# Kernel optimization log

Measured on AMD Instinct MI355X. Metric: run time of the kernel, lower is better.

## Reference

```python
import jax, jax.numpy as jnp
import numpy as np

RES = 2048
IN = 3
OUT = 2
THRESHOLD = 1.0
BETA = 0.9
SPECTRAL_RADIUS = 0.9


def _make_W(rng):
    # random recurrent matrix scaled to target spectral radius (power iteration estimate)
    W = rng.standard_normal((RES, RES)).astype(np.float32)
    v = rng.standard_normal(RES).astype(np.float32)
    lam = 1.0
    for _ in range(100):
        v = W @ v
        lam = np.linalg.norm(v)
        v = v / (lam + 1e-12)
    return W * (SPECTRAL_RADIUS / lam)


def _xavier(rng, fan_out, fan_in):
    bound = np.sqrt(6.0 / (fan_in + fan_out))
    return rng.uniform(-bound, bound, (fan_out, fan_in)).astype(np.float32)


def setup_inputs() -> dict:
    key = jax.random.key(0)
    rng = np.random.default_rng(42)
    x = jax.random.normal(key, (200, 256, IN), dtype=jnp.float32)
    W = jnp.asarray(_make_W(rng))            # [RES, RES] recurrent weights
    Win = jnp.asarray(_xavier(rng, RES, IN))  # [RES, IN]  input_layer.weight
    Wout = jnp.asarray(_xavier(rng, OUT, RES))  # [OUT, RES] readout.weight
    return {"x": x, "W": W, "Win": Win, "Wout": Wout}


def reference(x, W, Win, Wout):
    seq_len, batch, _ = x.shape
    res = W.shape[0]

    def step(carry, x_t):
        V, S = carry
        # leaky integrate: input current + recurrent current
        V_new = BETA * V + x_t @ Win.T + S @ W  # [batch, res]
        S_new = (V_new >= THRESHOLD).astype(V.dtype)
        V_new = V_new * (1.0 - S_new)  # reset_mechanism == 'zero'
        return (V_new, S_new), S_new

    init = (jnp.zeros((batch, res), x.dtype), jnp.zeros((batch, res), x.dtype))
    _, spk_rec = jax.lax.scan(step, init, x)  # [seq, batch, res]
    spk_avg = spk_rec[-10:].mean(axis=0)       # [batch, res]
    logits = spk_avg @ Wout.T                  # [batch, out]
    return spk_rec, logits
```

## Files before the change

kernel.cpp:

```cpp
#include <hip/hip_runtime.h>


#define SEQ    200
#define BATCH  256
#define NRES   2048
#define NTHR   1024
#define BETA_F 0.9f

__global__ __launch_bounds__(NTHR, 1) void snn_reservoir_kernel(
    const float* __restrict__ x,
    const float* __restrict__ W,
    const float* __restrict__ Win,
    const float* __restrict__ Wout,
    float* __restrict__ out)
{
    const int b    = blockIdx.x;
    const int tid  = threadIdx.x;
    const int lane = tid & 63;
    const int wid  = tid >> 6;
    const int n0   = tid << 1;

    __shared__ unsigned long long smask[2][32];
    __shared__ int   scum[2];
    __shared__ float4 sx[SEQ];
    __shared__ float red[2][16];

    for (int t = tid; t < SEQ; t += NTHR) {
        const float* p = x + (size_t)t * (BATCH * 3) + b * 3;
        sx[t] = make_float4(p[0], p[1], p[2], 0.0f);
    }
    if (tid < 64) smask[tid >> 5][tid & 31] = 0ull;
    if (tid < 2)  scum[tid] = 0;

    const float* wr = Win + (size_t)n0 * 3;
    const float w00 = wr[0], w01 = wr[1], w02 = wr[2];
    const float w10 = wr[3], w11 = wr[4], w12 = wr[5];

    float V0 = 0.f, V1 = 0.f;
    int cnt0 = 0, cnt1 = 0;

    __syncthreads();

    auto step = [&](int t, int cur, int prev, int& seen) {
        float rec0 = 0.f, rec1 = 0.f;
        const int c = scum[prev];
        if (__builtin_expect(c != seen, 0)) {
            seen = c;
            #pragma unroll 1
            for (int u = 0; u < 32; ++u) {
                unsigned long long m = smask[prev][u];
                const int kbase = ((u >> 1) << 7) + (u & 1);
                while (m) {
                    const int l = __builtin_ctzll(m);
                    m &= m - 1;
                    const int k = kbase + (l << 1);
                    const float2 wv = *(const float2*)(W + (size_t)k * NRES + n0);
                    rec0 += wv.x;
                    rec1 += wv.y;
                }
            }
        }
        const float4 xv = sx[t];
        const float i0 = fmaf(xv.x, w00, fmaf(xv.y, w01, xv.z * w02)) + rec0;
        const float i1 = fmaf(xv.x, w10, fmaf(xv.y, w11, xv.z * w12)) + rec1;
        V0 = fmaf(BETA_F, V0, i0);
        V1 = fmaf(BETA_F, V1, i1);
        const bool s0 = (V0 >= 1.0f);
        const bool s1 = (V1 >= 1.0f);
        V0 = s0 ? 0.f : V0;
        V1 = s1 ? 0.f : V1;
        *(float2*)(out + ((size_t)t * BATCH + b) * NRES + n0) =
            make_float2(s0 ? 1.f : 0.f, s1 ? 1.f : 0.f);
        if (t >= SEQ - 10) { cnt0 += (int)s0; cnt1 += (int)s1; }
        const unsigned long long b0 = __ballot(s0);
        const unsigned long long b1 = __ballot(s1);
        if (lane == 0) {
            smask[cur][2 * wid]     = b0;
            smask[cur][2 * wid + 1] = b1;
            const int pc = __popcll(b0) + __popcll(b1);
            if (pc) atomicAdd(&scum[cur], pc);
        }
        asm volatile("s_waitcnt lgkmcnt(0)\n\ts_barrier" ::: "memory");
    };

    int seen0 = 0, seen1 = 0;
    for (int tt = 0; tt < SEQ; tt += 2) {
        step(tt,     0, 1, seen1);
        step(tt + 1, 1, 0, seen0);
    }

    const float a0 = (float)cnt0 * 0.1f;
    const float a1 = (float)cnt1 * 0.1f;
    float p0 = fmaf(a0, Wout[n0], a1 * Wout[n0 + 1]);
    float p1 = fmaf(a0, Wout[NRES + n0], a1 * Wout[NRES + n0 + 1]);
    #pragma unroll
    for (int off = 32; off > 0; off >>= 1) {
        p0 += __shfl_down(p0, off);
        p1 += __shfl_down(p1, off);
    }
    if (lane == 0) { red[0][wid] = p0; red[1][wid] = p1; }
    __syncthreads();
    if (tid == 0) {
        float q0 = 0.f, q1 = 0.f;
        #pragma unroll
        for (int i = 0; i < 16; ++i) { q0 += red[0][i]; q1 += red[1][i]; }
        const size_t loff = (size_t)SEQ * BATCH * NRES;
        out[loff + b * 2 + 0] = q0;
        out[loff + b * 2 + 1] = q1;
    }
}

extern "C" void kernel_launch(void* const* d_in, const int* in_sizes, int n_in,
                              void* d_out, int out_size, void* d_ws, size_t ws_size,
                              hipStream_t stream) {
    const float* x    = (const float*)d_in[0];
    const float* W    = (const float*)d_in[1];
    const float* Win  = (const float*)d_in[2];
    const float* Wout = (const float*)d_in[3];
    float* out = (float*)d_out;
    hipLaunchKernelGGL(snn_reservoir_kernel, dim3(BATCH), dim3(NTHR), 0, stream,
                       x, W, Win, Wout, out);
}
```

Before: 410.2 us.

## Add barrier-free speculative no-spike pass with fallback to full recurrent simulation

Each block first runs the whole sequence ignoring recurrence, with no per-step barriers. This is exact as long as no neuron ever spikes, because the recurrent term is then zero. If any spike occurs, a block-wide flag triggers a re-run of the full simulation with per-step ballots, atomics and barriers, and it overwrites the output. Each thread now handles 4 neurons with float4 stores and gathers, on 512 threads per block. The aim is to remove the 200 per-step barriers when inputs never drive the membrane over threshold, at the cost of doing the work twice when they do.

```diff
diff --git a/kernel.cpp b/kernel.cpp
--- a/kernel.cpp
+++ b/kernel.cpp
@@ -4,7 +4,7 @@
 #define SEQ    200
 #define BATCH  256
 #define NRES   2048
-#define NTHR   1024
+#define NTHR   512
 #define BETA_F 0.9f
 
 __global__ __launch_bounds__(NTHR, 1) void snn_reservoir_kernel(
@@ -18,81 +18,125 @@
     const int tid  = threadIdx.x;
     const int lane = tid & 63;
     const int wid  = tid >> 6;
-    const int n0   = tid << 1;
+    const int n0   = tid << 2;
 
+    __shared__ float4 sx[SEQ];
     __shared__ unsigned long long smask[2][32];
     __shared__ int   scum[2];
-    __shared__ float4 sx[SEQ];
-    __shared__ float red[2][16];
+    __shared__ float red[2][8];
+    __shared__ int   anyflag;
 
     for (int t = tid; t < SEQ; t += NTHR) {
         const float* p = x + (size_t)t * (BATCH * 3) + b * 3;
         sx[t] = make_float4(p[0], p[1], p[2], 0.0f);
     }
-    if (tid < 64) smask[tid >> 5][tid & 31] = 0ull;
-    if (tid < 2)  scum[tid] = 0;
+    if (tid == 0) anyflag = 0;
 
-    const float* wr = Win + (size_t)n0 * 3;
-    const float w00 = wr[0], w01 = wr[1], w02 = wr[2];
-    const float w10 = wr[3], w11 = wr[4], w12 = wr[5];
+    float wi[4][3];
+    #pragma unroll
+    for (int j = 0; j < 4; ++j) {
+        const float* p = Win + (size_t)(n0 + j) * 3;
+        wi[j][0] = p[0]; wi[j][1] = p[1]; wi[j][2] = p[2];
+    }
 
-    float V0 = 0.f, V1 = 0.f;
-    int cnt0 = 0, cnt1 = 0;
+    float V[4]  = {0.f, 0.f, 0.f, 0.f};
+    int   cnt[4] = {0, 0, 0, 0};
 
     __syncthreads();
 
-    auto step = [&](int t, int cur, int prev, int& seen) {
-        float rec0 = 0.f, rec1 = 0.f;
-        const int c = scum[prev];
-        if (__builtin_expect(c != seen, 0)) {
-            seen = c;
-            #pragma unroll 1
-            for (int u = 0; u < 32; ++u) {
-                unsigned long long m = smask[prev][u];
-                const int kbase = ((u >> 1) << 7) + (u & 1);
-                while (m) {
-                    const int l = __builtin_ctzll(m);
-                    m &= m - 1;
-                    const int k = kbase + (l << 1);
-                    const float2 wv = *(const float2*)(W + (size_t)k * NRES + n0);
-                    rec0 += wv.x;
-                    rec1 += wv.y;
+    {
+        float* po = out + (size_t)b * NRES + n0;
+        bool spiked = false;
+        #pragma unroll 2
+        for (int t = 0; t < SEQ; ++t) {
+            const float4 xv = sx[t];
+            float4 sp;
+            #pragma unroll
+            for (int j = 0; j < 4; ++j) {
+                const float cur = fmaf(xv.x, wi[j][0],
+                                  fmaf(xv.y, wi[j][1], xv.z * wi[j][2]));
+                V[j] = fmaf(BETA_F, V[j], cur);
+                const bool s = (V[j] >= 1.0f);
+                spiked |= s;
+                V[j] = s ? 0.f : V[j];
+                ((float*)&sp)[j] = s ? 1.f : 0.f;
+                if (t >= SEQ - 10) cnt[j] += (int)s;
+            }
+            *(float4*)po = sp;
+            po += BATCH * NRES;
+        }
+        const unsigned long long bal = __ballot(spiked);
+        if (lane == 0 && bal != 0ull) atomicOr(&anyflag, 1);
+    }
+    __syncthreads();
+
+    if (anyflag) {
+        #pragma unroll
+        for (int j = 0; j < 4; ++j) { V[j] = 0.f; cnt[j] = 0; }
+        if (tid < 64) smask[tid >> 5][tid & 31] = 0ull;
+        if (tid < 2)  scum[tid] = 0;
+        __syncthreads();
+
+        int seen[2] = {0, 0};
+        float* po = out + (size_t)b * NRES + n0;
+        for (int t = 0; t < SEQ; ++t) {
+            const int curp = t & 1, prev = curp ^ 1;
+            float rec[4] = {0.f, 0.f, 0.f, 0.f};
+            const int c = scum[prev];
+            if (c != seen[prev]) {
+                seen[prev] = c;
+                #pragma unroll 1
+                for (int u = 0; u < 32; ++u) {
+                    unsigned long long m = smask[prev][u];
+                    const int kbase = ((u >> 2) << 8) + (u & 3);
+                    while (m) {
+                        const int l = __builtin_ctzll(m);
+                        m &= m - 1;
+                        const int k = kbase + (l << 2);
+                        const float4 wv = *(const float4*)(W + (size_t)k * NRES + n0);
+                        rec[0] += wv.x; rec[1] += wv.y;
+                        rec[2] += wv.z; rec[3] += wv.w;
+                    }
                 }
             }
+            const float4 xv = sx[t];
+            float4 sp;
+            int pc = 0;
+            unsigned long long bj[4];
+            #pragma unroll
+            for (int j = 0; j < 4; ++j) {
+                const float cur = fmaf(xv.x, wi[j][0],
+                                  fmaf(xv.y, wi[j][1], xv.z * wi[j][2])) + rec[j];
+                V[j] = fmaf(BETA_F, V[j], cur);
+                const bool s = (V[j] >= 1.0f);
+                V[j] = s ? 0.f : V[j];
+                ((float*)&sp)[j] = s ? 1.f : 0.f;
+                if (t >= SEQ - 10) cnt[j] += (int)s;
+                bj[j] = __ballot(s);
+                pc += (int)s;
+            }
+            *(float4*)po = sp;
+            po += BATCH * NRES;
+            if (lane == 0) {
+                #pragma unroll
+                for (int j = 0; j < 4; ++j) smask[curp][(wid << 2) + j] = bj[j];
+            }
+            if (lane == 0) {
+                int wpc = 0;
+                #pragma unroll
+                for (int j = 0; j < 4; ++j) wpc += __popcll(bj[j]);
+                if (wpc) atomicAdd(&scum[curp], wpc);
+            }
+            __syncthreads();
         }
-        const float4 xv = sx[t];
-        const float i0 = fmaf(xv.x, w00, fmaf(xv.y, w01, xv.z * w02)) + rec0;
-        const float i1 = fmaf(xv.x, w10, fmaf(xv.y, w11, xv.z * w12)) + rec1;
-        V0 = fmaf(BETA_F, V0, i0);
-        V1 = fmaf(BETA_F, V1, i1);
-        const bool s0 = (V0 >= 1.0f);
-        const bool s1 = (V1 >= 1.0f);
-        V0 = s0 ? 0.f : V0;
-        V1 = s1 ? 0.f : V1;
-        *(float2*)(out + ((size_t)t * BATCH + b) * NRES + n0) =
-            make_float2(s0 ? 1.f : 0.f, s1 ? 1.f : 0.f);
-        if (t >= SEQ - 10) { cnt0 += (int)s0; cnt1 += (int)s1; }
-        const unsigned long long b0 = __ballot(s0);
-        const unsigned long long b1 = __ballot(s1);
-        if (lane == 0) {
-            smask[cur][2 * wid]     = b0;
-            smask[cur][2 * wid + 1] = b1;
-            const int pc = __popcll(b0) + __popcll(b1);
-            if (pc) atomicAdd(&scum[cur], pc);
-        }
-        asm volatile("s_waitcnt lgkmcnt(0)\n\ts_barrier" ::: "memory");
-    };
-
-    int seen0 = 0, seen1 = 0;
-    for (int tt = 0; tt < SEQ; tt += 2) {
-        step(tt,     0, 1, seen1);
-        step(tt + 1, 1, 0, seen0);
     }
 
-    const float a0 = (float)cnt0 * 0.1f;
-    const float a1 = (float)cnt1 * 0.1f;
-    float p0 = fmaf(a0, Wout[n0], a1 * Wout[n0 + 1]);
-    float p1 = fmaf(a0, Wout[NRES + n0], a1 * Wout[NRES + n0 + 1]);
+    const float4 w0 = *(const float4*)(Wout + n0);
+    const float4 w1 = *(const float4*)(Wout + NRES + n0);
+    float p0 = cnt[0] * 0.1f * w0.x + cnt[1] * 0.1f * w0.y +
+               cnt[2] * 0.1f * w0.z + cnt[3] * 0.1f * w0.w;
+    float p1 = cnt[0] * 0.1f * w1.x + cnt[1] * 0.1f * w1.y +
+               cnt[2] * 0.1f * w1.z + cnt[3] * 0.1f * w1.w;
     #pragma unroll
     for (int off = 32; off > 0; off >>= 1) {
         p0 += __shfl_down(p0, off);
@@ -103,7 +147,7 @@
     if (tid == 0) {
         float q0 = 0.f, q1 = 0.f;
         #pragma unroll
-        for (int i = 0; i < 16; ++i) { q0 += red[0][i]; q1 += red[1][i]; }
+        for (int i = 0; i < 8; ++i) { q0 += red[0][i]; q1 += red[1][i]; }
         const size_t loff = (size_t)SEQ * BATCH * NRES;
         out[loff + b * 2 + 0] = q0;
         out[loff + b * 2 + 1] = q1;
```

New measurement: 423.7 us. +3.3%, slower.

## Add barrier-free speculative no-spike pass with fallback to full recurrent loop

Applied to the files above, without the earlier changes.

Runs a first pass that ignores the recurrent term, updates the membrane potentials with no per-step barrier and writes spikes with nontemporal stores. The recurrent contribution is only nonzero once some neuron has spiked, so if no thread in the block ever spikes this pass is exact. A block-wide flag detects any spike, and in that case the block reruns the original barrier-synchronised recurrent simulation from scratch. This removes 200 block barriers per step loop in the common no-spike case, at the cost of doubling the work and output writes for blocks that do spike.

```diff
diff --git a/kernel.cpp b/kernel.cpp
--- a/kernel.cpp
+++ b/kernel.cpp
@@ -6,6 +6,8 @@
 #define NRES   2048
 #define NTHR   1024
 #define BETA_F 0.9f
+
+typedef float f2_t __attribute__((ext_vector_type(2)));
 
 __global__ __launch_bounds__(NTHR, 1) void snn_reservoir_kernel(
     const float* __restrict__ x,
@@ -20,17 +22,17 @@
     const int wid  = tid >> 6;
     const int n0   = tid << 1;
 
+    __shared__ float4 sx[SEQ];
     __shared__ unsigned long long smask[2][32];
     __shared__ int   scum[2];
-    __shared__ float4 sx[SEQ];
     __shared__ float red[2][16];
+    __shared__ int   anyflag;
 
     for (int t = tid; t < SEQ; t += NTHR) {
         const float* p = x + (size_t)t * (BATCH * 3) + b * 3;
         sx[t] = make_float4(p[0], p[1], p[2], 0.0f);
     }
-    if (tid < 64) smask[tid >> 5][tid & 31] = 0ull;
-    if (tid < 2)  scum[tid] = 0;
+    if (tid == 0) anyflag = 0;
 
     const float* wr = Win + (size_t)n0 * 3;
     const float w00 = wr[0], w01 = wr[1], w02 = wr[2];
@@ -41,52 +43,87 @@
 
     __syncthreads();
 
-    auto step = [&](int t, int cur, int prev, int& seen) {
-        float rec0 = 0.f, rec1 = 0.f;
-        const int c = scum[prev];
-        if (__builtin_expect(c != seen, 0)) {
-            seen = c;
-            #pragma unroll 1
-            for (int u = 0; u < 32; ++u) {
-                unsigned long long m = smask[prev][u];
-                const int kbase = ((u >> 1) << 7) + (u & 1);
-                while (m) {
-                    const int l = __builtin_ctzll(m);
-                    m &= m - 1;
-                    const int k = kbase + (l << 1);
-                    const float2 wv = *(const float2*)(W + (size_t)k * NRES + n0);
-                    rec0 += wv.x;
-                    rec1 += wv.y;
+    {
+        float* po = out + (size_t)b * NRES + n0;
+        bool spiked = false;
+        #pragma unroll 4
+        for (int t = 0; t < SEQ - 10; ++t) {
+            const float4 xv = sx[t];
+            V0 = fmaf(BETA_F, V0, fmaf(xv.x, w00, fmaf(xv.y, w01, xv.z * w02)));
+            V1 = fmaf(BETA_F, V1, fmaf(xv.x, w10, fmaf(xv.y, w11, xv.z * w12)));
+            const bool s0 = (V0 >= 1.0f), s1 = (V1 >= 1.0f);
+            spiked |= (s0 | s1);
+            V0 = s0 ? 0.f : V0;
+            V1 = s1 ? 0.f : V1;
+            f2_t sp; sp[0] = s0 ? 1.f : 0.f; sp[1] = s1 ? 1.f : 0.f;
+            __builtin_nontemporal_store(sp, (f2_t*)po);
+            po += BATCH * NRES;
+        }
+        #pragma unroll
+        for (int t = SEQ - 10; t < SEQ; ++t) {
+            const float4 xv = sx[t];
+            V0 = fmaf(BETA_F, V0, fmaf(xv.x, w00, fmaf(xv.y, w01, xv.z * w02)));
+            V1 = fmaf(BETA_F, V1, fmaf(xv.x, w10, fmaf(xv.y, w11, xv.z * w12)));
+            const bool s0 = (V0 >= 1.0f), s1 = (V1 >= 1.0f);
+            spiked |= (s0 | s1);
+            cnt0 += (int)s0; cnt1 += (int)s1;
+            V0 = s0 ? 0.f : V0;
+            V1 = s1 ? 0.f : V1;
+            f2_t sp; sp[0] = s0 ? 1.f : 0.f; sp[1] = s1 ? 1.f : 0.f;
+            __builtin_nontemporal_store(sp, (f2_t*)po);
+            po += BATCH * NRES;
+        }
+        const unsigned long long bal = __ballot(spiked);
+        if (lane == 0 && bal != 0ull) atomicOr(&anyflag, 1);
+    }
+    __syncthreads();
+
+    if (anyflag) {
+        V0 = 0.f; V1 = 0.f; cnt0 = 0; cnt1 = 0;
+        if (tid < 64) smask[tid >> 5][tid & 31] = 0ull;
+        if (tid < 2)  scum[tid] = 0;
+        __syncthreads();
+
+        int seen[2] = {0, 0};
+        float* po = out + (size_t)b * NRES + n0;
+        for (int t = 0; t < SEQ; ++t) {
+            const int curp = t & 1, prev = curp ^ 1;
+            float rec0 = 0.f, rec1 = 0.f;
+            const int c = scum[prev];
+            if (c != seen[prev]) {
+                seen[prev] = c;
+                #pragma unroll 1
+                for (int u = 0; u < 32; ++u) {
+                    unsigned long long m = smask[prev][u];
+                    const int kbase = ((u >> 1) << 7) + (u & 1);
+                    while (m) {
+                        const int l = __builtin_ctzll(m);
+                        m &= m - 1;
+                        const int k = kbase + (l << 1);
+                        const float2 wv = *(const float2*)(W + (size_t)k * NRES + n0);
+                        rec0 += wv.x; rec1 += wv.y;
+                    }
                 }
             }
+            const float4 xv = sx[t];
+            V0 = fmaf(BETA_F, V0, fmaf(xv.x, w00, fmaf(xv.y, w01, xv.z * w02)) + rec0);
+            V1 = fmaf(BETA_F, V1, fmaf(xv.x, w10, fmaf(xv.y, w11, xv.z * w12)) + rec1);
+            const bool s0 = (V0 >= 1.0f), s1 = (V1 >= 1.0f);
+            V0 = s0 ? 0.f : V0;
+            V1 = s1 ? 0.f : V1;
+            *(float2*)po = make_float2(s0 ? 1.f : 0.f, s1 ? 1.f : 0.f);
+            po += BATCH * NRES;
+            if (t >= SEQ - 10) { cnt0 += (int)s0; cnt1 += (int)s1; }
+            const unsigned long long b0 = __ballot(s0);
+            const unsigned long long b1 = __ballot(s1);
+            if (lane == 0) {
+                smask[curp][2 * wid]     = b0;
+                smask[curp][2 * wid + 1] = b1;
+                const int pc = __popcll(b0) + __popcll(b1);
+                if (pc) atomicAdd(&scum[curp], pc);
+            }
+            __syncthreads();
         }
-        const float4 xv = sx[t];
-        const float i0 = fmaf(xv.x, w00, fmaf(xv.y, w01, xv.z * w02)) + rec0;
-        const float i1 = fmaf(xv.x, w10, fmaf(xv.y, w11, xv.z * w12)) + rec1;
-        V0 = fmaf(BETA_F, V0, i0);
-        V1 = fmaf(BETA_F, V1, i1);
-        const bool s0 = (V0 >= 1.0f);
-        const bool s1 = (V1 >= 1.0f);
-        V0 = s0 ? 0.f : V0;
-        V1 = s1 ? 0.f : V1;
-        *(float2*)(out + ((size_t)t * BATCH + b) * NRES + n0) =
-            make_float2(s0 ? 1.f : 0.f, s1 ? 1.f : 0.f);
-        if (t >= SEQ - 10) { cnt0 += (int)s0; cnt1 += (int)s1; }
-        const unsigned long long b0 = __ballot(s0);
-        const unsigned long long b1 = __ballot(s1);
-        if (lane == 0) {
-            smask[cur][2 * wid]     = b0;
-            smask[cur][2 * wid + 1] = b1;
-            const int pc = __popcll(b0) + __popcll(b1);
-            if (pc) atomicAdd(&scum[cur], pc);
-        }
-        asm volatile("s_waitcnt lgkmcnt(0)\n\ts_barrier" ::: "memory");
-    };
-
-    int seen0 = 0, seen1 = 0;
-    for (int tt = 0; tt < SEQ; tt += 2) {
-        step(tt,     0, 1, seen1);
-        step(tt + 1, 1, 0, seen0);
     }
 
     const float a0 = (float)cnt0 * 0.1f;
```

Result: slower. 426.5 us (+4.0%).
